# Performance work log

Measured on AMD Instinct MI355X. Metric: run time of the kernel, lower is better.

The kernel has to match this reference:

```python
import jax, jax.numpy as jnp
import numpy as np

TOPK_RATIO = 0.2
ALIGN_WEIGHT = 1.0
REG_WEIGHT = 0.1
EPS_LN = 1e-6
EPS_COS = 1e-8


def setup_inputs() -> dict:
    key = jax.random.key(0)
    k1, k2, k3, k4, k5 = jax.random.split(key, 5)
    B, C, H, W = 8, 256, 200, 200
    return {
        "bev_map": jax.random.normal(k1, (B, C, H, W), dtype=jnp.float32),
        "prior_warp": jax.random.normal(k2, (B, C, H, W), dtype=jnp.float32),
        "dx_m": jax.random.normal(k3, (B,), dtype=jnp.float32),
        "dy_m": jax.random.normal(k4, (B,), dtype=jnp.float32),
        "dtheta": jax.random.normal(k5, (B,), dtype=jnp.float32),
    }


def _channel_layer_norm(x):
    # per-pixel mean/std over channel dim; torch std is unbiased (ddof=1)
    mu = jnp.mean(x, axis=1, keepdims=True)
    sigma = jnp.std(x, axis=1, keepdims=True, ddof=1) + EPS_LN
    return (x - mu) / sigma


def reference(bev_map, prior_warp, dx_m, dy_m, dtheta):
    B, C, H, W = bev_map.shape
    bev_norm = _channel_layer_norm(bev_map)      # [B,C,H,W]
    prior_norm = _channel_layer_norm(prior_warp)  # [B,C,H,W]

    # squared-sum score per pixel, flattened over spatial dims
    score = jnp.sum(bev_map * bev_map, axis=1).reshape(B, H * W)  # [B,HW]
    k = max(1, int(TOPK_RATIO * H * W))
    _, idx = jax.lax.top_k(score, k)             # [B,k]

    idx_bc = jnp.broadcast_to(idx[:, None, :], (B, C, k))
    bev_topk = jnp.take_along_axis(bev_norm.reshape(B, C, H * W), idx_bc, axis=2)
    prior_topk = jnp.take_along_axis(prior_norm.reshape(B, C, H * W), idx_bc, axis=2)

    # cosine similarity over channel dim (torch eps semantics: clamp each norm)
    num = jnp.sum(bev_topk * prior_topk, axis=1)                       # [B,k]
    na = jnp.sqrt(jnp.sum(bev_topk * bev_topk, axis=1))
    nb = jnp.sqrt(jnp.sum(prior_topk * prior_topk, axis=1))
    sim = num / (jnp.maximum(na, EPS_COS) * jnp.maximum(nb, EPS_COS))
    align_loss = jnp.mean(1.0 - sim)

    reg_loss = jnp.mean(dx_m * dx_m + dy_m * dy_m) + jnp.mean(dtheta * dtheta)
    return ALIGN_WEIGHT * align_loss + REG_WEIGHT * reg_loss
```

## Files before the change

kernel.cpp:

```cpp
#include <hip/hip_runtime.h>
#include <math.h>

#define BATCH 8
#define CCH 256
#define HW 40000
#define HW4 (HW / 4)
#define KSEL 8000
#define EPS_LN 1e-6f
#define EPS_COS 1e-8f
#define SLICES 40
#define SLICE_LEN (HW / SLICES)

#define OFF_SCORE   0
#define OFF_CONTRIB 320000
#define OFF_HIST1   640000
#define OFF_HIST2   1164288
#define OFF_PREFIX  1688576
#define OFF_REM1    1688584
#define OFF_TKEY    1688592
#define OFF_REM2    1688600
#define OFF_TIE     1688608
#define OFF_BSUMS   1688616

__device__ __forceinline__ unsigned int mono_key(float x) {
  unsigned int u = __float_as_uint(x);
  return (u & 0x80000000u) ? ~u : (u | 0x80000000u);
}

__global__ __launch_bounds__(256) void zero_kernel(unsigned int* __restrict__ ws) {
  const int n4 = (2 * BATCH * 65536) / 4;
  uint4* p = (uint4*)(ws + OFF_HIST1);
  uint4 z = {0u, 0u, 0u, 0u};
  for (int i = blockIdx.x * blockDim.x + threadIdx.x; i < n4; i += gridDim.x * blockDim.x)
    p[i] = z;
  if (blockIdx.x == 0 && threadIdx.x < BATCH) ws[OFF_BSUMS + threadIdx.x] = 0u;
}

__global__ __launch_bounds__(256) void pixel_stats_kernel(
    const float* __restrict__ A, const float* __restrict__ B,
    float* __restrict__ score, float* __restrict__ contrib) {
  int tid = blockIdx.x * blockDim.x + threadIdx.x;
  if (tid >= BATCH * HW4) return;
  int b = tid / HW4;
  int p4 = tid - b * HW4;
  const float4* a  = (const float4*)(A + (size_t)b * CCH * HW) + p4;
  const float4* bb = (const float4*)(B + (size_t)b * CCH * HW) + p4;

  float sa[4] = {0, 0, 0, 0}, ssa[4] = {0, 0, 0, 0};
  float sb[4] = {0, 0, 0, 0}, ssb[4] = {0, 0, 0, 0}, dab[4] = {0, 0, 0, 0};
#pragma unroll 4
  for (int c = 0; c < CCH; ++c) {
    float4 x = a[(size_t)c * HW4];
    float4 y = bb[(size_t)c * HW4];
    float xs[4] = {x.x, x.y, x.z, x.w};
    float ys[4] = {y.x, y.y, y.z, y.w};
#pragma unroll
    for (int j = 0; j < 4; ++j) {
      sa[j] += xs[j];
      ssa[j] = fmaf(xs[j], xs[j], ssa[j]);
      sb[j] += ys[j];
      ssb[j] = fmaf(ys[j], ys[j], ssb[j]);
      dab[j] = fmaf(xs[j], ys[j], dab[j]);
    }
  }

  float scv[4], cov[4];
  const float invC = 1.0f / (float)CCH;
#pragma unroll
  for (int j = 0; j < 4; ++j) {
    scv[j] = ssa[j];
    float mua = sa[j] * invC, mub = sb[j] * invC;
    float cssa = fmaxf(ssa[j] - (float)CCH * mua * mua, 0.f);
    float cssb = fmaxf(ssb[j] - (float)CCH * mub * mub, 0.f);
    float cdot = dab[j] - (float)CCH * mua * mub;
    float siga = sqrtf(cssa / (float)(CCH - 1)) + EPS_LN;
    float sigb = sqrtf(cssb / (float)(CCH - 1)) + EPS_LN;
    float num = cdot / (siga * sigb);
    float na = sqrtf(cssa) / siga;
    float nb = sqrtf(cssb) / sigb;
    cov[j] = 1.0f - num / (fmaxf(na, EPS_COS) * fmaxf(nb, EPS_COS));
  }
  int out = b * HW + p4 * 4;
  *(float4*)(score + out)   = make_float4(scv[0], scv[1], scv[2], scv[3]);
  *(float4*)(contrib + out) = make_float4(cov[0], cov[1], cov[2], cov[3]);
}

__global__ __launch_bounds__(256) void hist1_kernel(
    const float* __restrict__ score, unsigned int* __restrict__ ws) {
  int b = blockIdx.x / SLICES;
  int sl = blockIdx.x - b * SLICES;
  const float* s = score + b * HW;
  unsigned int* h = ws + OFF_HIST1 + (b << 16);
  int base = sl * SLICE_LEN;
  for (int i = base + threadIdx.x; i < base + SLICE_LEN; i += 256) {
    unsigned int key = mono_key(s[i]);
    atomicAdd(&h[key >> 16], 1u);
  }
}

__global__ __launch_bounds__(256) void hist2_kernel(
    const float* __restrict__ score, unsigned int* __restrict__ ws) {
  int b = blockIdx.x / SLICES;
  int sl = blockIdx.x - b * SLICES;
  const float* s = score + b * HW;
  unsigned int pref = ws[OFF_PREFIX + b];
  unsigned int* h = ws + OFF_HIST2 + (b << 16);
  int base = sl * SLICE_LEN;
  for (int i = base + threadIdx.x; i < base + SLICE_LEN; i += 256) {
    unsigned int key = mono_key(s[i]);
    if ((key >> 16) == pref) atomicAdd(&h[key & 0xFFFFu], 1u);
  }
}

__global__ __launch_bounds__(1024) void select_kernel(unsigned int* __restrict__ ws,
                                                      int phase) {
  int b = blockIdx.x;
  const unsigned int* h = ws + (phase ? OFF_HIST2 : OFF_HIST1) + (b << 16);
  unsigned int K = phase ? ws[OFF_REM1 + b] : (unsigned int)KSEL;

  __shared__ unsigned int chunk[1024];
  __shared__ unsigned int suf[1024];
  __shared__ unsigned int s_chunk_idx, s_cum_above;
  __shared__ unsigned int bins[64];

  int t = threadIdx.x;
  unsigned int sum = 0;
#pragma unroll 8
  for (int i = 0; i < 64; ++i) sum += h[t * 64 + i];
  chunk[t] = sum;
  suf[t] = sum;
  __syncthreads();
  for (int off = 1; off < 1024; off <<= 1) {
    unsigned int v = (t + off < 1024) ? suf[t + off] : 0u;
    __syncthreads();
    suf[t] += v;
    __syncthreads();
  }
  unsigned int above = (t == 1023) ? 0u : suf[t + 1];
  if (suf[t] >= K && above < K) { s_chunk_idx = (unsigned int)t; s_cum_above = above; }
  __syncthreads();
  if (t < 64) bins[t] = h[s_chunk_idx * 64 + t];
  __syncthreads();
  if (t == 0) {
    unsigned int cum = s_cum_above;
    int d = 63;
    for (; d >= 0; --d) {
      if (cum + bins[d] >= K) break;
      cum += bins[d];
    }
    unsigned int binidx = s_chunk_idx * 64 + (unsigned int)d;
    if (phase == 0) {
      ws[OFF_PREFIX + b] = binidx;
      ws[OFF_REM1 + b] = K - cum;
    } else {
      ws[OFF_TKEY + b] = (ws[OFF_PREFIX + b] << 16) | binidx;
      ws[OFF_REM2 + b] = K - cum;
      ws[OFF_TIE + b] = 0u;
    }
  }
}

__global__ __launch_bounds__(256) void sum_kernel(
    const float* __restrict__ score, const float* __restrict__ contrib,
    unsigned int* __restrict__ ws) {
  int b = blockIdx.x / SLICES;
  int sl = blockIdx.x - b * SLICES;
  const float* s = score + b * HW;
  const float* ct = contrib + b * HW;
  unsigned int T = ws[OFF_TKEY + b];
  unsigned int rem2 = ws[OFF_REM2 + b];

  float partial = 0.f;
  int base = sl * SLICE_LEN;
  for (int i = base + threadIdx.x; i < base + SLICE_LEN; i += 256) {
    unsigned int key = mono_key(s[i]);
    if (key > T) {
      partial += ct[i];
    } else if (key == T) {
      unsigned int old = atomicAdd(&ws[OFF_TIE + b], 1u);
      if (old < rem2) partial += ct[i];
    }
  }

  __shared__ float red[256];
  red[threadIdx.x] = partial;
  __syncthreads();
  for (int off = 128; off > 0; off >>= 1) {
    if (threadIdx.x < (unsigned)off) red[threadIdx.x] += red[threadIdx.x + off];
    __syncthreads();
  }
  if (threadIdx.x == 0) atomicAdd((float*)(ws + OFF_BSUMS) + b, red[0]);
}

__global__ void finalize_kernel(const unsigned int* __restrict__ ws,
                                const float* __restrict__ dx,
                                const float* __restrict__ dy,
                                const float* __restrict__ dth,
                                float* __restrict__ out) {
  if (threadIdx.x == 0 && blockIdx.x == 0) {
    const float* bsums = (const float*)(ws + OFF_BSUMS);
    float s = 0.f;
    for (int b = 0; b < BATCH; ++b) s += bsums[b];
    float align = s / (float)(BATCH * KSEL);
    float r1 = 0.f, r2 = 0.f;
    for (int b = 0; b < BATCH; ++b) {
      r1 += dx[b] * dx[b] + dy[b] * dy[b];
      r2 += dth[b] * dth[b];
    }
    out[0] = align + 0.1f * (r1 / (float)BATCH + r2 / (float)BATCH);
  }
}

extern "C" void kernel_launch(void* const* d_in, const int* in_sizes, int n_in,
                              void* d_out, int out_size, void* d_ws, size_t ws_size,
                              hipStream_t stream) {
  const float* bev   = (const float*)d_in[0];
  const float* prior = (const float*)d_in[1];
  const float* dx    = (const float*)d_in[2];
  const float* dy    = (const float*)d_in[3];
  const float* dth   = (const float*)d_in[4];
  float* out = (float*)d_out;

  unsigned int* ws = (unsigned int*)d_ws;
  float* score   = (float*)ws + OFF_SCORE;
  float* contrib = (float*)ws + OFF_CONTRIB;

  zero_kernel<<<256, 256, 0, stream>>>(ws);
  pixel_stats_kernel<<<(BATCH * HW4 + 255) / 256, 256, 0, stream>>>(bev, prior, score, contrib);
  hist1_kernel<<<BATCH * SLICES, 256, 0, stream>>>(score, ws);
  select_kernel<<<BATCH, 1024, 0, stream>>>(ws, 0);
  hist2_kernel<<<BATCH * SLICES, 256, 0, stream>>>(score, ws);
  select_kernel<<<BATCH, 1024, 0, stream>>>(ws, 1);
  sum_kernel<<<BATCH * SLICES, 256, 0, stream>>>(score, contrib, ws);
  finalize_kernel<<<1, 64, 0, stream>>>(ws, dx, dy, dth, out);
}
```

Baseline: 708.3 us.

## Fuse first histogram into pixel stats and use nontemporal vector loads

The first-pass radix histogram is now built inside the pixel statistics kernel using the freshly computed scores, which removes the separate hist1 kernel launch and its reread of the score array. The channel loop switches to nontemporal vector loads and a deeper unroll, so the streamed inputs are meant to bypass cache retention. The cost is added global atomics at the tail of the bandwidth-bound kernel, which could contend on popular histogram bins.

```diff
diff --git a/kernel.cpp b/kernel.cpp
--- a/kernel.cpp
+++ b/kernel.cpp
@@ -22,6 +22,8 @@
 #define OFF_TIE     1688608
 #define OFF_BSUMS   1688616
 
+typedef float v4f __attribute__((ext_vector_type(4)));
+
 __device__ __forceinline__ unsigned int mono_key(float x) {
   unsigned int u = __float_as_uint(x);
   return (u & 0x80000000u) ? ~u : (u | 0x80000000u);
@@ -38,29 +40,29 @@
 
 __global__ __launch_bounds__(256) void pixel_stats_kernel(
     const float* __restrict__ A, const float* __restrict__ B,
-    float* __restrict__ score, float* __restrict__ contrib) {
+    float* __restrict__ score, float* __restrict__ contrib,
+    unsigned int* __restrict__ ws) {
   int tid = blockIdx.x * blockDim.x + threadIdx.x;
   if (tid >= BATCH * HW4) return;
   int b = tid / HW4;
   int p4 = tid - b * HW4;
-  const float4* a  = (const float4*)(A + (size_t)b * CCH * HW) + p4;
-  const float4* bb = (const float4*)(B + (size_t)b * CCH * HW) + p4;
+  const v4f* a  = (const v4f*)(A + (size_t)b * CCH * HW) + p4;
+  const v4f* bb = (const v4f*)(B + (size_t)b * CCH * HW) + p4;
 
   float sa[4] = {0, 0, 0, 0}, ssa[4] = {0, 0, 0, 0};
   float sb[4] = {0, 0, 0, 0}, ssb[4] = {0, 0, 0, 0}, dab[4] = {0, 0, 0, 0};
-#pragma unroll 4
+#pragma unroll 8
   for (int c = 0; c < CCH; ++c) {
-    float4 x = a[(size_t)c * HW4];
-    float4 y = bb[(size_t)c * HW4];
-    float xs[4] = {x.x, x.y, x.z, x.w};
-    float ys[4] = {y.x, y.y, y.z, y.w};
+    v4f x = __builtin_nontemporal_load(a + (size_t)c * HW4);
+    v4f y = __builtin_nontemporal_load(bb + (size_t)c * HW4);
 #pragma unroll
     for (int j = 0; j < 4; ++j) {
-      sa[j] += xs[j];
-      ssa[j] = fmaf(xs[j], xs[j], ssa[j]);
-      sb[j] += ys[j];
-      ssb[j] = fmaf(ys[j], ys[j], ssb[j]);
-      dab[j] = fmaf(xs[j], ys[j], dab[j]);
+      float xs = x[j], ys = y[j];
+      sa[j] += xs;
+      ssa[j] = fmaf(xs, xs, ssa[j]);
+      sb[j] += ys;
+      ssb[j] = fmaf(ys, ys, ssb[j]);
+      dab[j] = fmaf(xs, ys, dab[j]);
     }
   }
 
@@ -81,21 +83,13 @@
     cov[j] = 1.0f - num / (fmaxf(na, EPS_COS) * fmaxf(nb, EPS_COS));
   }
   int out = b * HW + p4 * 4;
-  *(float4*)(score + out)   = make_float4(scv[0], scv[1], scv[2], scv[3]);
-  *(float4*)(contrib + out) = make_float4(cov[0], cov[1], cov[2], cov[3]);
-}
-
-__global__ __launch_bounds__(256) void hist1_kernel(
-    const float* __restrict__ score, unsigned int* __restrict__ ws) {
-  int b = blockIdx.x / SLICES;
-  int sl = blockIdx.x - b * SLICES;
-  const float* s = score + b * HW;
-  unsigned int* h = ws + OFF_HIST1 + (b << 16);
-  int base = sl * SLICE_LEN;
-  for (int i = base + threadIdx.x; i < base + SLICE_LEN; i += 256) {
-    unsigned int key = mono_key(s[i]);
-    atomicAdd(&h[key >> 16], 1u);
-  }
+  *(v4f*)(score + out)   = (v4f){scv[0], scv[1], scv[2], scv[3]};
+  *(v4f*)(contrib + out) = (v4f){cov[0], cov[1], cov[2], cov[3]};
+
+  unsigned int* h1 = ws + OFF_HIST1 + (b << 16);
+#pragma unroll
+  for (int j = 0; j < 4; ++j)
+    atomicAdd(&h1[mono_key(scv[j]) >> 16], 1u);
 }
 
 __global__ __launch_bounds__(256) void hist2_kernel(
@@ -226,8 +220,7 @@
   float* contrib = (float*)ws + OFF_CONTRIB;
 
   zero_kernel<<<256, 256, 0, stream>>>(ws);
-  pixel_stats_kernel<<<(BATCH * HW4 + 255) / 256, 256, 0, stream>>>(bev, prior, score, contrib);
-  hist1_kernel<<<BATCH * SLICES, 256, 0, stream>>>(score, ws);
+  pixel_stats_kernel<<<(BATCH * HW4 + 255) / 256, 256, 0, stream>>>(bev, prior, score, contrib, ws);
   select_kernel<<<BATCH, 1024, 0, stream>>>(ws, 0);
   hist2_kernel<<<BATCH * SLICES, 256, 0, stream>>>(score, ws);
   select_kernel<<<BATCH, 1024, 0, stream>>>(ws, 1);
```

After: 710.5 us. About the same (+0.3%).
